# Optimization experiments

Measured on AMD Instinct MI355X. Metric: run time of the kernel, lower is better.

## Reference

```python
import jax, jax.numpy as jnp
import numpy as np

# ---------- spherical offset pattern (setup-time, numpy, exact port) ----------

def _get_xy(dp, dt):
    t, c = np.tan, np.cos
    return np.array([
        [(-t(dt), 1/c(dt)*t(dp)), (0, t(dp)), (t(dt), 1/c(dt)*t(dp))],
        [(-t(dt), 0),             (1, 1),     (t(dt), 0)],
        [(-t(dt), -1/c(dt)*t(dp)), (0, -t(dp)), (t(dt), -1/c(dt)*t(dp))]])


def _cal_offset(h, w, r, c):
    phi = -((r + 0.5) / h * np.pi - np.pi / 2)
    theta = (c + 0.5) / w * 2 * np.pi - np.pi
    xys = _get_xy(np.pi / h, 2 * np.pi / w)
    x, y = xys[..., 0], xys[..., 1]
    rho = np.sqrt(x ** 2 + y ** 2)
    v = np.arctan(rho)
    new_phi = np.arcsin(np.cos(v) * np.sin(phi) + y * np.sin(v) * np.cos(phi) / rho)
    new_theta = theta + np.arctan(x * np.sin(v) / (rho * np.cos(phi) * np.cos(v) - y * np.sin(phi) * np.sin(v)))
    new_r = (-new_phi + np.pi / 2) * h / np.pi - 0.5
    new_c = (new_theta + np.pi) * w / 2 / np.pi - 0.5
    new_c = (new_c + w) % w
    res = np.stack([new_r, new_c], axis=-1)
    res[1, 1] = (r, c)
    for i in range(3):
        for j in range(3):
            res[i, j, 0] -= (r + i - 1)
            res[i, j, 1] -= (c + j - 1)
    return res.reshape(-1)  # (18,) ordered k=i*3+j, pairs (dy, dx)


def _offsets_map(h, w):
    with np.errstate(all='ignore'):
        co = np.array([[_cal_offset(h, w, i, j) for j in range(w)] for i in range(h)])
    return co.transpose(2, 0, 1)  # (18, h, w)


# ---------- jax forward ----------

def _bilinear_gather(x, py, px):
    # x: [B,C,H,W]; py/px: [K,H,W] float sample coords. Zero padding outside.
    B, C, H, W = x.shape
    y0 = jnp.floor(py); x0 = jnp.floor(px)
    wy = py - y0; wx = px - x0
    y0i = y0.astype(jnp.int32); x0i = x0.astype(jnp.int32)
    xf = x.reshape(B, C, H * W)

    def corner(yi, xi, wgt):
        valid = (yi >= 0) & (yi < H) & (xi >= 0) & (xi < W)
        idx = (jnp.clip(yi, 0, H - 1) * W + jnp.clip(xi, 0, W - 1)).reshape(-1)
        v = jnp.take(xf, idx, axis=2).reshape(B, C, *py.shape)  # [B,C,K,H,W]
        return v * (wgt * valid.astype(x.dtype))[None, None]

    return (corner(y0i,     x0i,     (1 - wy) * (1 - wx)) +
            corner(y0i,     x0i + 1, (1 - wy) * wx) +
            corner(y0i + 1, x0i,     wy * (1 - wx)) +
            corner(y0i + 1, x0i + 1, wy * wx))


def _forward(x, weight, bias, w_down, w_up, scale, offset):
    B, C, H, W = x.shape
    O = weight.shape[0]
    # frozen dense 3x3 conv (stride 1, pad 1)
    h = jax.lax.conv_general_dilated(
        x, weight, window_strides=(1, 1), padding=((1, 1), (1, 1)),
        dimension_numbers=('NCHW', 'OIHW', 'NCHW'))
    h = h + bias[None, :, None, None]
    # deform_conv2d with fixed spherical offsets (offset: [18,H,W] -> [9,2,H,W])
    off = offset.reshape(9, 2, H, W)
    dy, dx_ = off[:, 0], off[:, 1]
    kk = jnp.arange(9)
    ki = (kk // 3).astype(x.dtype); kj = (kk % 3).astype(x.dtype)
    pp = jnp.arange(H, dtype=x.dtype); qq = jnp.arange(W, dtype=x.dtype)
    py = pp[None, :, None] - 1.0 + ki[:, None, None] + dy  # [9,H,W]
    px = qq[None, None, :] - 1.0 + kj[:, None, None] + dx_
    sampled = _bilinear_gather(x, py, px)                   # [B,C,9,H,W]
    dconv = jnp.einsum('bckhw,ock->bohw', sampled, weight.reshape(O, C, 9))
    dconv = dconv + bias[None, :, None, None]
    # concat + dual 1x1 conv LoRA fusion + scaled residual
    cat = jnp.concatenate([dconv, h], axis=1)               # [B,2O,H,W]
    down = jnp.einsum('bchw,oc->bohw', cat, w_down)
    up = jnp.einsum('bchw,oc->bohw', down, w_up)
    return h + scale * up


def setup_inputs() -> dict:
    key = jax.random.key(0)
    ks = jax.random.split(key, 6)
    B, C, O, H, W = 4, 320, 320, 64, 64
    low = max(O // 1, 1)
    x = jax.random.normal(ks[0], (B, C, H, W), dtype=jnp.float32)
    weight = jax.random.normal(ks[1], (O, C, 3, 3), dtype=jnp.float32) * 0.02
    bias = jax.random.normal(ks[2], (O,), dtype=jnp.float32) * 0.02
    w_down = jax.random.normal(ks[3], (low, 2 * O), dtype=jnp.float32) * 0.02
    w_up = jax.random.normal(ks[4], (O, low), dtype=jnp.float32) * 0.02
    scale = jnp.asarray(1.0, dtype=jnp.float32)
    offset = jnp.asarray(_offsets_map(H, W), dtype=jnp.float32)  # [18,H,W]
    return {'x': x, 'weight': weight, 'bias': bias, 'w_down': w_down,
            'w_up': w_up, 'scale': scale, 'offset': offset}


def reference(x, weight, bias, w_down, w_up, scale, offset):
    return _forward(x, weight, bias, w_down, w_up, scale, offset)
```

## Files before the change

kernel.cpp:

```cpp
#include <hip/hip_runtime.h>
#include <stdint.h>


typedef __attribute__((ext_vector_type(4))) float f32x4;
typedef __attribute__((ext_vector_type(8))) short bf16x8;

typedef __attribute__((address_space(1))) const unsigned int uint_as1;
typedef __attribute__((address_space(3))) unsigned int uint_as3;

__device__ __forceinline__ void gl_lds16(const void* g, void* l) {
    __builtin_amdgcn_global_load_lds((uint_as1*)g, (uint_as3*)l, 16, 0, 0);
}

__device__ __forceinline__ unsigned short f2b(float f) {
    union { float f; uint32_t u; } v; v.f = f;
    uint32_t r = (v.u + 0x7FFFu + ((v.u >> 16) & 1u)) >> 16;
    return (unsigned short)r;
}
__device__ __forceinline__ float b2f(unsigned short h) {
    union { uint32_t u; float f; } v; v.u = ((uint32_t)h) << 16;
    return v.f;
}
__device__ __forceinline__ float b2f_lo(uint32_t u) {
    union { uint32_t u; float f; } v; v.u = u << 16;
    return v.f;
}
__device__ __forceinline__ float b2f_hi(uint32_t u) {
    union { uint32_t u; float f; } v; v.u = u & 0xFFFF0000u;
    return v.f;
}
__device__ __forceinline__ uint32_t pack2(float lo, float hi) {
    return (uint32_t)f2b(lo) | ((uint32_t)f2b(hi) << 16);
}

#define TAP8(AC, tv, wvx) \
    AC[0] += wvx * b2f_lo((uint32_t)tv.x); AC[1] += wvx * b2f_hi((uint32_t)tv.x); \
    AC[2] += wvx * b2f_lo((uint32_t)tv.y); AC[3] += wvx * b2f_hi((uint32_t)tv.y); \
    AC[4] += wvx * b2f_lo((uint32_t)tv.z); AC[5] += wvx * b2f_hi((uint32_t)tv.z); \
    AC[6] += wvx * b2f_lo((uint32_t)tv.w); AC[7] += wvx * b2f_hi((uint32_t)tv.w);

__global__ __launch_bounds__(256) void k_prep(const float* __restrict__ off,
                                              const float* __restrict__ w,
                                              const float* __restrict__ wd,
                                              const float* __restrict__ wu,
                                              const float* __restrict__ x,
                                              uint32_t* __restrict__ oIdx,
                                              float* __restrict__ oW,
                                              unsigned short* __restrict__ Wr2,
                                              unsigned short* __restrict__ W2,
                                              unsigned short* __restrict__ Xb)
{
    const int bx = blockIdx.x, tid = threadIdx.x;
    if (bx < 144) {
        int gid = bx * 256 + tid;
        int k = gid >> 12;
        int p = gid & 4095;
        int i = p >> 6, j = p & 63;
        float dy = off[(2 * k) * 4096 + p];
        float dx = off[(2 * k + 1) * 4096 + p];
        float py = (float)(i - 1 + k / 3) + dy;
        float px = (float)(j - 1 + k % 3) + dx;
        float fy = floorf(py), fx = floorf(px);
        float wy = py - fy, wx = px - fx;
        fy = fminf(fmaxf(fy, -100.f), 100.f);
        fx = fminf(fmaxf(fx, -100.f), 100.f);
        int y0 = (int)fy, x0 = (int)fx;
        float vy0 = (y0 >= 0 && y0 < 64) ? 1.f : 0.f;
        float vy1 = (y0 >= -1 && y0 < 63) ? 1.f : 0.f;
        float vx0 = (x0 >= 0 && x0 < 64) ? 1.f : 0.f;
        float vx1 = (x0 >= -1 && x0 < 63) ? 1.f : 0.f;
        float w00 = (1.f - wy) * (1.f - wx) * vy0 * vx0;
        float w01 = (1.f - wy) * wx * vy0 * vx1;
        float w10 = wy * (1.f - wx) * vy1 * vx0;
        float w11 = wy * wx * vy1 * vx1;
        int ya = min(max(y0, 0), 63), yb = min(max(y0 + 1, 0), 63);
        int xa = min(max(x0, 0), 63), xb = min(max(x0 + 1, 0), 63);
        oIdx[gid * 2 + 0] = (uint32_t)(ya * 64 + xa) | ((uint32_t)(ya * 64 + xb) << 16);
        oIdx[gid * 2 + 1] = (uint32_t)(yb * 64 + xa) | ((uint32_t)(yb * 64 + xb) << 16);
        oW[gid * 4 + 0] = w00;
        oW[gid * 4 + 1] = w01;
        oW[gid * 4 + 2] = w10;
        oW[gid * 4 + 3] = w11;
    } else if (bx < 594) {
        int gid = (bx - 144) * 256 + tid;
        int cb = gid / 2880, m = gid - cb * 2880;
        int k = m / 320, o = m - k * 320;
        float v[8];
        #pragma unroll
        for (int cl = 0; cl < 8; ++cl) {
            int c = cb * 8 + cl;
            v[cl] = w[((size_t)o * 320 + c) * 9 + k];
        }
        int4 st;
        st.x = (int)pack2(v[0], v[1]);
        st.y = (int)pack2(v[2], v[3]);
        st.z = (int)pack2(v[4], v[5]);
        st.w = (int)pack2(v[6], v[7]);
        *(int4*)(Wr2 + (size_t)gid * 8) = st;
    } else if (bx < 1554) {
        int gid = (bx - 594) * 256 + tid;
        int o = gid / 640, kk2 = gid % 640;
        float a0 = 0.f, a1 = 0.f, a2 = 0.f, a3 = 0.f;
        if (o < 320) {
            const float* wuo = wu + (size_t)o * 320;
            for (int l = 0; l < 320; l += 4) {
                float4 u4 = *(const float4*)(wuo + l);
                a0 += u4.x * wd[(size_t)(l + 0) * 640 + kk2];
                a1 += u4.y * wd[(size_t)(l + 1) * 640 + kk2];
                a2 += u4.z * wd[(size_t)(l + 2) * 640 + kk2];
                a3 += u4.w * wd[(size_t)(l + 3) * 640 + kk2];
            }
        }
        W2[(size_t)((kk2 >> 3) * 384 + o) * 8 + (kk2 & 7)] = f2b((a0 + a1) + (a2 + a3));
    } else {
        int bz = bx - 1554;
        int sp = bz & 3, rest = bz >> 2;
        int gl = rest % 40, b = rest / 40;
        const float* xb = x + ((size_t)b * 320 + gl * 8) * 4096;
        unsigned short* xpb = Xb + ((size_t)gl * 16384 + b * 4096) * 8;
        #pragma unroll
        for (int i = 0; i < 4; ++i) {
            int px = sp * 1024 + i * 256 + tid;
            float v0 = xb[0 * 4096 + px], v1 = xb[1 * 4096 + px];
            float v2 = xb[2 * 4096 + px], v3 = xb[3 * 4096 + px];
            float v4 = xb[4 * 4096 + px], v5 = xb[5 * 4096 + px];
            float v6 = xb[6 * 4096 + px], v7 = xb[7 * 4096 + px];
            int4 st;
            st.x = (int)pack2(v0, v1);
            st.y = (int)pack2(v2, v3);
            st.z = (int)pack2(v4, v5);
            st.w = (int)pack2(v6, v7);
            *(int4*)(xpb + (size_t)px * 8) = st;
        }
    }
}

__global__ __launch_bounds__(256, 3) void k_zgemm(const unsigned short* __restrict__ Xb,
                                                  const unsigned short* __restrict__ Wr2,
                                                  unsigned short* __restrict__ Z)
{
    __shared__ __align__(16) unsigned short Bs[2][8 * 128 * 8];
    const int tid = threadIdx.x;
    const int n0 = blockIdx.x * 128, m0 = blockIdx.y * 160;
    const int lane = tid & 63, w = tid >> 6;
    const int wm = w & 1, wn = w >> 1;
    const int quad = lane >> 4, nl = lane & 15;
    const unsigned short* Abase = Wr2 + ((size_t)quad * 2880 + m0 + wm * 80 + nl) * 8;

#define STAGE_B(buf, s1) do { \
    _Pragma("unroll") \
    for (int q_ = 0; q_ < 4; ++q_) { \
        int u_ = tid + q_ * 256; \
        int row_ = u_ >> 7, nn_ = n0 + (u_ & 127); \
        gl_lds16(Xb + ((size_t)((s1) * 8 + row_) * 16384 + nn_) * 8, &Bs[buf][u_ * 8]); \
    } \
} while (0)

    f32x4 acc[5][4];
    #pragma unroll
    for (int mt = 0; mt < 5; ++mt)
        #pragma unroll
        for (int nt = 0; nt < 4; ++nt)
            acc[mt][nt] = 0.f;

    STAGE_B(0, 0);
    asm volatile("s_waitcnt vmcnt(0)" ::: "memory");
    __builtin_amdgcn_s_barrier();
    __builtin_amdgcn_sched_barrier(0);

    for (int s = 0; s < 5; ++s) {
        const int p = s & 1, np = p ^ 1;
        bf16x8 a[2][5];
        #pragma unroll
        for (int kc = 0; kc < 2; ++kc)
            #pragma unroll
            for (int mt = 0; mt < 5; ++mt)
                a[kc][mt] = *(const bf16x8*)(Abase
                    + ((size_t)((s * 8 + kc * 4) * 2880) + mt * 16) * 8);
        if (s < 4) STAGE_B(np, s + 1);
        __builtin_amdgcn_sched_barrier(0);
        #pragma unroll
        for (int kc = 0; kc < 2; ++kc) {
            bf16x8 bf[4];
            #pragma unroll
            for (int nt = 0; nt < 4; ++nt)
                bf[nt] = *(const bf16x8*)&Bs[p][((kc * 4 + quad) * 128 + wn * 64 + nt * 16 + nl) * 8];
            #pragma unroll
            for (int mt = 0; mt < 5; ++mt)
                #pragma unroll
                for (int nt = 0; nt < 4; ++nt)
                    acc[mt][nt] = __builtin_amdgcn_mfma_f32_16x16x32_bf16(a[kc][mt], bf[nt], acc[mt][nt], 0, 0, 0);
        }
        asm volatile("s_waitcnt vmcnt(0)" ::: "memory");
        __builtin_amdgcn_s_barrier();
        __builtin_amdgcn_sched_barrier(0);
    }

    #pragma unroll
    for (int mt = 0; mt < 5; ++mt) {
        int o0m = m0 + wm * 80 + mt * 16 + quad * 4;
        #pragma unroll
        for (int nt = 0; nt < 4; ++nt) {
            int n2 = n0 + wn * 64 + nt * 16 + nl;
            unsigned short* pp = Z + ((size_t)(o0m >> 3) * 16384 + n2) * 8 + (o0m & 7);
            ushort4 st;
            st.x = f2b(acc[mt][nt][0]);
            st.y = f2b(acc[mt][nt][1]);
            st.z = f2b(acc[mt][nt][2]);
            st.w = f2b(acc[mt][nt][3]);
            *(ushort4*)pp = st;
        }
    }
#undef STAGE_B
}

__global__ __launch_bounds__(256) void k_blend(const unsigned short* __restrict__ Z,
                                               const uint32_t* __restrict__ oIdx,
                                               const float* __restrict__ oW,
                                               const float* __restrict__ bias,
                                               unsigned short* __restrict__ Cc)
{
    const int tid = threadIdx.x;
    const int px = blockIdx.x * 256 + tid;
    const int og = blockIdx.y;
    const int b = blockIdx.z;
    const int r = px >> 6, c0 = px & 63;

    float ac[8], ah[8];
    {
        float4 b0 = *(const float4*)&bias[og * 8];
        float4 b1 = *(const float4*)&bias[og * 8 + 4];
        ac[0] = b0.x; ac[1] = b0.y; ac[2] = b0.z; ac[3] = b0.w;
        ac[4] = b1.x; ac[5] = b1.y; ac[6] = b1.z; ac[7] = b1.w;
        #pragma unroll
        for (int j = 0; j < 8; ++j) ah[j] = ac[j];
    }
    #pragma unroll
    for (int k = 0; k < 9; ++k) {
        int gi = (k << 12) + px;
        uint32_t i0 = oIdx[gi * 2];
        uint32_t i1 = oIdx[gi * 2 + 1];
        float4 wv = *(const float4*)&oW[(size_t)gi * 4];
        int rr = r + k / 3 - 1, cc = c0 + k % 3 - 1;
        bool valid = (rr >= 0) & (rr < 64) & (cc >= 0) & (cc < 64);
        int hidx = valid ? (rr * 64 + cc) : 0;
        float hw = valid ? 1.f : 0.f;
        const unsigned short* Zb = Z + ((size_t)(k * 40 + og) * 16384 + b * 4096) * 8;
        int4 t0 = *(const int4*)(Zb + (size_t)(i0 & 0xFFFFu) * 8);
        int4 t1 = *(const int4*)(Zb + (size_t)(i0 >> 16) * 8);
        int4 t2 = *(const int4*)(Zb + (size_t)(i1 & 0xFFFFu) * 8);
        int4 t3 = *(const int4*)(Zb + (size_t)(i1 >> 16) * 8);
        int4 th = *(const int4*)(Zb + (size_t)hidx * 8);
        TAP8(ac, t0, wv.x) TAP8(ac, t1, wv.y)
        TAP8(ac, t2, wv.z) TAP8(ac, t3, wv.w)
        TAP8(ah, th, hw)
    }
    int4 sd, sh;
    sd.x = (int)pack2(ac[0], ac[1]); sd.y = (int)pack2(ac[2], ac[3]);
    sd.z = (int)pack2(ac[4], ac[5]); sd.w = (int)pack2(ac[6], ac[7]);
    sh.x = (int)pack2(ah[0], ah[1]); sh.y = (int)pack2(ah[2], ah[3]);
    sh.z = (int)pack2(ah[4], ah[5]); sh.w = (int)pack2(ah[6], ah[7]);
    unsigned short* cp = Cc + ((size_t)og * 32768 + b * 4096 + px) * 8;
    *(int4*)cp = sd;
    *(int4*)(cp + 16384 * 8) = sh;
}

__global__ __launch_bounds__(256) void k_final(const unsigned short* __restrict__ W2,
                                               const unsigned short* __restrict__ Cc,
                                               const float* __restrict__ scale,
                                               float* __restrict__ out)
{
    __shared__ __align__(16) unsigned short As[2][8 * 160 * 8];
    __shared__ __align__(16) unsigned short Bs[2][8 * 64 * 8];
    const int tid = threadIdx.x;
    const int n0 = blockIdx.x * 64, m0 = blockIdx.y * 160;
    const int lane = tid & 63, w = tid >> 6;
    const int wm = w & 1, wn = w >> 1;
    const int quad = lane >> 4, nl = lane & 15;

#define STAGEF(buf, s1) do { \
    _Pragma("unroll") \
    for (int q_ = 0; q_ < 5; ++q_) { \
        int u_ = tid + q_ * 256; \
        int kq_ = u_ / 160, m_ = u_ - kq_ * 160; \
        gl_lds16(W2 + ((size_t)(((s1) * 8 + kq_) * 384 + m0 + m_)) * 8, &As[buf][u_ * 8]); \
    } \
    { \
        int h_off_ = ((s1) < 5) ? 0 : 16384; \
        int gq_ = ((s1) < 5) ? (s1) * 8 : ((s1) - 5) * 8; \
        _Pragma("unroll") \
        for (int q_ = 0; q_ < 2; ++q_) { \
            int u_ = tid + q_ * 256; \
            int row_ = u_ >> 6, nn_ = n0 + (u_ & 63); \
            gl_lds16(Cc + ((size_t)(gq_ + row_) * 32768 + h_off_ + nn_) * 8, &Bs[buf][u_ * 8]); \
        } \
    } \
} while (0)

    f32x4 acc[5][2];
    #pragma unroll
    for (int mt = 0; mt < 5; ++mt)
        #pragma unroll
        for (int nt = 0; nt < 2; ++nt)
            acc[mt][nt] = 0.f;

    STAGEF(0, 0);
    asm volatile("s_waitcnt vmcnt(0)" ::: "memory");
    __builtin_amdgcn_s_barrier();
    __builtin_amdgcn_sched_barrier(0);

    for (int s = 0; s < 10; ++s) {
        const int p = s & 1, np = p ^ 1;
        if (s < 9) STAGEF(np, s + 1);
        __builtin_amdgcn_sched_barrier(0);
        #pragma unroll
        for (int kc = 0; kc < 2; ++kc) {
            bf16x8 a[5], bf[2];
            #pragma unroll
            for (int mt = 0; mt < 5; ++mt)
                a[mt] = *(const bf16x8*)&As[p][((kc * 4 + quad) * 160 + wm * 80 + mt * 16 + nl) * 8];
            #pragma unroll
            for (int nt = 0; nt < 2; ++nt)
                bf[nt] = *(const bf16x8*)&Bs[p][((kc * 4 + quad) * 64 + wn * 32 + nt * 16 + nl) * 8];
            #pragma unroll
            for (int mt = 0; mt < 5; ++mt)
                #pragma unroll
                for (int nt = 0; nt < 2; ++nt)
                    acc[mt][nt] = __builtin_amdgcn_mfma_f32_16x16x32_bf16(a[mt], bf[nt], acc[mt][nt], 0, 0, 0);
        }
        asm volatile("s_waitcnt vmcnt(0)" ::: "memory");
        __builtin_amdgcn_s_barrier();
        __builtin_amdgcn_sched_barrier(0);
    }

    float sc = scale[0];
    #pragma unroll
    for (int mt = 0; mt < 5; ++mt) {
        int o0 = m0 + wm * 80 + mt * 16 + quad * 4;
        #pragma unroll
        for (int nt = 0; nt < 2; ++nt) {
            int n = n0 + wn * 32 + nt * 16 + nl;
            int b = n >> 12, px = n & 4095;
            ushort4 hv = *(const ushort4*)(Cc + ((size_t)(o0 >> 3) * 32768 + n + 16384) * 8 + (o0 & 7));
            size_t base = ((size_t)(b * 320 + o0)) * 4096 + px;
            out[base]            = b2f(hv.x) + sc * acc[mt][nt][0];
            out[base + 4096]     = b2f(hv.y) + sc * acc[mt][nt][1];
            out[base + 2 * 4096] = b2f(hv.z) + sc * acc[mt][nt][2];
            out[base + 3 * 4096] = b2f(hv.w) + sc * acc[mt][nt][3];
        }
    }
#undef STAGEF
}

extern "C" void kernel_launch(void* const* d_in, const int* in_sizes, int n_in,
                              void* d_out, int out_size, void* d_ws, size_t ws_size,
                              hipStream_t stream)
{
    const float* x      = (const float*)d_in[0];
    const float* weight = (const float*)d_in[1];
    const float* bias   = (const float*)d_in[2];
    const float* w_down = (const float*)d_in[3];
    const float* w_up   = (const float*)d_in[4];
    const float* scale  = (const float*)d_in[5];
    const float* offset = (const float*)d_in[6];
    char* ws = (char*)d_ws;
    unsigned short* Cc    = (unsigned short*)(ws + 0);
    unsigned short* Wr2   = (unsigned short*)(ws + 25165824);
    unsigned short* W2    = (unsigned short*)(ws + 27377664);
    uint32_t*       oI    = (uint32_t*)(ws + 27869184);
    float*          oWt   = (float*)(ws + 28164096);
    unsigned short* Xb    = (unsigned short*)(ws + 28758016);
    unsigned short* Z     = (unsigned short*)(ws + 39909376);
    float* out = (float*)d_out;

    hipLaunchKernelGGL(k_prep, dim3(2194), dim3(256), 0, stream,
                       offset, weight, w_down, w_up, x, oI, oWt, Wr2, W2, Xb);
    hipLaunchKernelGGL(k_zgemm, dim3(128, 18), dim3(256), 0, stream,
                       Xb, Wr2, Z);
    hipLaunchKernelGGL(k_blend, dim3(16, 40, 4), dim3(256), 0, stream,
                       Z, oI, oWt, bias, Cc);
    hipLaunchKernelGGL(k_final, dim3(256, 2), dim3(256), 0, stream,
                       W2, Cc, scale, out);
}
```

Before: 178.0 us.

## Stage each Z plane in LDS for blend gathers instead of global loads

After: 216.1 us. 21.4% more time.

```diff
diff --git a/kernel.cpp b/kernel.cpp
--- a/kernel.cpp
+++ b/kernel.cpp
@@ -214,55 +214,77 @@
 #undef STAGE_B
 }
 
-__global__ __launch_bounds__(256) void k_blend(const unsigned short* __restrict__ Z,
+__global__ __launch_bounds__(512) void k_blend(const unsigned short* __restrict__ Z,
                                                const uint32_t* __restrict__ oIdx,
                                                const float* __restrict__ oW,
                                                const float* __restrict__ bias,
                                                unsigned short* __restrict__ Cc)
 {
+    __shared__ __align__(16) unsigned short Zp[4096 * 8];
     const int tid = threadIdx.x;
-    const int px = blockIdx.x * 256 + tid;
-    const int og = blockIdx.y;
-    const int b = blockIdx.z;
-    const int r = px >> 6, c0 = px & 63;
-
-    float ac[8], ah[8];
+    const int sp = blockIdx.x, og = blockIdx.y, b = blockIdx.z;
+    const int px0 = sp * 1024;
+
+    float ac[2][8], ah[2][8];
     {
         float4 b0 = *(const float4*)&bias[og * 8];
         float4 b1 = *(const float4*)&bias[og * 8 + 4];
-        ac[0] = b0.x; ac[1] = b0.y; ac[2] = b0.z; ac[3] = b0.w;
-        ac[4] = b1.x; ac[5] = b1.y; ac[6] = b1.z; ac[7] = b1.w;
-        #pragma unroll
-        for (int j = 0; j < 8; ++j) ah[j] = ac[j];
-    }
+        #pragma unroll
+        for (int j = 0; j < 2; ++j) {
+            ac[j][0] = b0.x; ac[j][1] = b0.y; ac[j][2] = b0.z; ac[j][3] = b0.w;
+            ac[j][4] = b1.x; ac[j][5] = b1.y; ac[j][6] = b1.z; ac[j][7] = b1.w;
+            #pragma unroll
+            for (int q = 0; q < 8; ++q) ah[j][q] = ac[j][q];
+        }
+    }
+
+    for (int k = 0; k < 9; ++k) {
+        const unsigned short* Zplane = Z + ((size_t)(k * 40 + og) * 16384 + b * 4096) * 8;
+        #pragma unroll
+        for (int q = 0; q < 8; ++q) {
+            int u = tid + q * 512;
+            gl_lds16(Zplane + (size_t)u * 8, &Zp[u * 8]);
+        }
+        asm volatile("s_waitcnt vmcnt(0)" ::: "memory");
+        __builtin_amdgcn_s_barrier();
+
+        #pragma unroll
+        for (int j = 0; j < 2; ++j) {
+            int lpx = j * 512 + tid;
+            int px = px0 + lpx;
+            int gi = (k << 12) + px;
+            uint32_t i0 = oIdx[gi * 2];
+            uint32_t i1 = oIdx[gi * 2 + 1];
+            float4 wv = *(const float4*)&oW[(size_t)gi * 4];
+            int r = px >> 6, c0 = px & 63;
+            int rr = r + k / 3 - 1, cc = c0 + k % 3 - 1;
+            bool valid = (rr >= 0) & (rr < 64) & (cc >= 0) & (cc < 64);
+            int hidx = valid ? (rr * 64 + cc) : 0;
+            float hw = valid ? 1.f : 0.f;
+            int4 t0 = *(const int4*)&Zp[(size_t)(i0 & 0xFFFFu) * 8];
+            int4 t1 = *(const int4*)&Zp[(size_t)(i0 >> 16) * 8];
+            int4 t2 = *(const int4*)&Zp[(size_t)(i1 & 0xFFFFu) * 8];
+            int4 t3 = *(const int4*)&Zp[(size_t)(i1 >> 16) * 8];
+            int4 th = *(const int4*)&Zp[(size_t)hidx * 8];
+            TAP8(ac[j], t0, wv.x) TAP8(ac[j], t1, wv.y)
+            TAP8(ac[j], t2, wv.z) TAP8(ac[j], t3, wv.w)
+            TAP8(ah[j], th, hw)
+        }
+        __builtin_amdgcn_s_barrier();
+    }
+
     #pragma unroll
-    for (int k = 0; k < 9; ++k) {
-        int gi = (k << 12) + px;
-        uint32_t i0 = oIdx[gi * 2];
-        uint32_t i1 = oIdx[gi * 2 + 1];
-        float4 wv = *(const float4*)&oW[(size_t)gi * 4];
-        int rr = r + k / 3 - 1, cc = c0 + k % 3 - 1;
-        bool valid = (rr >= 0) & (rr < 64) & (cc >= 0) & (cc < 64);
-        int hidx = valid ? (rr * 64 + cc) : 0;
-        float hw = valid ? 1.f : 0.f;
-        const unsigned short* Zb = Z + ((size_t)(k * 40 + og) * 16384 + b * 4096) * 8;
-        int4 t0 = *(const int4*)(Zb + (size_t)(i0 & 0xFFFFu) * 8);
-        int4 t1 = *(const int4*)(Zb + (size_t)(i0 >> 16) * 8);
-        int4 t2 = *(const int4*)(Zb + (size_t)(i1 & 0xFFFFu) * 8);
-        int4 t3 = *(const int4*)(Zb + (size_t)(i1 >> 16) * 8);
-        int4 th = *(const int4*)(Zb + (size_t)hidx * 8);
-        TAP8(ac, t0, wv.x) TAP8(ac, t1, wv.y)
-        TAP8(ac, t2, wv.z) TAP8(ac, t3, wv.w)
-        TAP8(ah, th, hw)
-    }
-    int4 sd, sh;
-    sd.x = (int)pack2(ac[0], ac[1]); sd.y = (int)pack2(ac[2], ac[3]);
-    sd.z = (int)pack2(ac[4], ac[5]); sd.w = (int)pack2(ac[6], ac[7]);
-    sh.x = (int)pack2(ah[0], ah[1]); sh.y = (int)pack2(ah[2], ah[3]);
-    sh.z = (int)pack2(ah[4], ah[5]); sh.w = (int)pack2(ah[6], ah[7]);
-    unsigned short* cp = Cc + ((size_t)og * 32768 + b * 4096 + px) * 8;
-    *(int4*)cp = sd;
-    *(int4*)(cp + 16384 * 8) = sh;
+    for (int j = 0; j < 2; ++j) {
+        int px = px0 + j * 512 + tid;
+        int4 sd, sh;
+        sd.x = (int)pack2(ac[j][0], ac[j][1]); sd.y = (int)pack2(ac[j][2], ac[j][3]);
+        sd.z = (int)pack2(ac[j][4], ac[j][5]); sd.w = (int)pack2(ac[j][6], ac[j][7]);
+        sh.x = (int)pack2(ah[j][0], ah[j][1]); sh.y = (int)pack2(ah[j][2], ah[j][3]);
+        sh.z = (int)pack2(ah[j][4], ah[j][5]); sh.w = (int)pack2(ah[j][6], ah[j][7]);
+        unsigned short* cp = Cc + ((size_t)og * 32768 + b * 4096 + px) * 8;
+        *(int4*)cp = sd;
+        *(int4*)(cp + 16384 * 8) = sh;
+    }
 }
 
 __global__ __launch_bounds__(256) void k_final(const unsigned short* __restrict__ W2,
@@ -377,7 +399,7 @@
                        offset, weight, w_down, w_up, x, oI, oWt, Wr2, W2, Xb);
     hipLaunchKernelGGL(k_zgemm, dim3(128, 18), dim3(256), 0, stream,
                        Xb, Wr2, Z);
-    hipLaunchKernelGGL(k_blend, dim3(16, 40, 4), dim3(256), 0, stream,
+    hipLaunchKernelGGL(k_blend, dim3(4, 40, 4), dim3(512), 0, stream,
                        Z, oI, oWt, bias, Cc);
     hipLaunchKernelGGL(k_final, dim3(256, 2), dim3(256), 0, stream,
                        W2, Cc, scale, out);
```
